# Optimization experiments

Measured on AMD Instinct MI355X. Metric: run time of the kernel, lower is better.

The kernel has to match this reference:

```python
import jax, jax.numpy as jnp
import numpy as np

MARGIN = 0.1

def setup_inputs() -> dict:
    key = jax.random.key(0)
    k1, k2 = jax.random.split(key)
    embeddings = jax.random.normal(k1, (8192, 128), dtype=jnp.float32)
    labels = jax.random.randint(k2, (8192,), 0, 64, dtype=jnp.int64)
    return {"embeddings": embeddings, "labels": labels}

def reference(embeddings, labels):
    # sim[i,j] = <e_i, e_j>
    sim = embeddings @ embeddings.T  # [n, n]
    eq = labels[:, None] == labels[None, :]  # pos mask (includes diagonal)
    # per entry: exp(margin - sim) for positives, exp(sim - margin) for negatives
    terms = jnp.where(eq, jnp.exp(MARGIN - sim), jnp.exp(sim - MARGIN))
    # loss_i = log(sum_j terms[i,j]); loss = mean_i loss_i
    return jnp.mean(jnp.log(jnp.sum(terms, axis=1)))
```

## Files before the change

kernel.cpp:

```cpp
#include <hip/hip_runtime.h>
#include <hip/hip_bf16.h>

#define N 8192
#define D 128
#define LOG2E  1.44269504088896f
#define LN2    0.69314718055995f

typedef __attribute__((ext_vector_type(8))) short bf16x8;
typedef __attribute__((ext_vector_type(4))) float f32x4;

#if __has_builtin(__builtin_amdgcn_exp2f)
#define EXP2(x) __builtin_amdgcn_exp2f(x)
#else
#define EXP2(x) exp2f(x)
#endif
#if __has_builtin(__builtin_amdgcn_logf)
#define LOG2(x) __builtin_amdgcn_logf(x)
#else
#define LOG2(x) log2f(x)
#endif

static __device__ __forceinline__ unsigned short f2bf(float f) {
    union { float f; unsigned int u; } x;
    x.f = f;
    unsigned int r = ((x.u >> 16) & 1u) + 0x7FFFu;
    return (unsigned short)((x.u + r) >> 16);
}

__global__ void prep_kernel(const float* __restrict__ E,
                            uint4* __restrict__ Eb2,
                            unsigned int* __restrict__ counter) {
    const int j = blockIdx.x * 256 + threadIdx.x;
    const int l  = j & 15;
    const int q  = (j >> 4) & 3;
    const int kk = (j >> 6) & 3;
    const int S  = j >> 8;
    const float4* src = (const float4*)(E + (size_t)(S * 16 + l) * D + kk * 32 + q * 8);
    float4 f0 = src[0], f1 = src[1];
    uint4 o;
    o.x = f2bf(f0.x) | ((unsigned)f2bf(f0.y) << 16);
    o.y = f2bf(f0.z) | ((unsigned)f2bf(f0.w) << 16);
    o.z = f2bf(f1.x) | ((unsigned)f2bf(f1.y) << 16);
    o.w = f2bf(f1.z) | ((unsigned)f2bf(f1.w) << 16);
    Eb2[j] = o;
    if (j == 0) *counter = 0u;
}

__global__ __launch_bounds__(256) void fused_kernel(
        const unsigned short* __restrict__ Eb2,
        const int* __restrict__ labels,
        float* __restrict__ part) {
    __shared__ int   labC[128];
    __shared__ int   labR[128];
    __shared__ float colacc[128];

    const int tid  = threadIdx.x;
    const int wid  = tid >> 6;
    const int lane = tid & 63;
    const int q = lane >> 4;
    const int l = lane & 15;

    const int b = blockIdx.x;
    int r = (int)(64.5f - sqrtf(64.5f * 64.5f - 2.0f * (float)b));
    while ((r + 1) * 64 - ((r + 1) * r) / 2 <= b) ++r;
    while (r * 64 - (r * (r - 1)) / 2 > b) --r;
    const int c = r + (b - (r * 64 - (r * (r - 1)) / 2));
    const bool diag = (r == c);
    const int tile_m0 = r * 128;
    const int n_begin = c * 128;
    const int mrow0 = wid * 32;

    const char* base = (const char*)Eb2;

    bf16x8 a[2][4];
#pragma unroll
    for (int g = 0; g < 2; ++g) {
        const char* pa = base + (size_t)(r * 8 + wid * 2 + g) * 4096 + lane * 16;
#pragma unroll
        for (int kk = 0; kk < 4; ++kk)
            a[g][kk] = *(const bf16x8*)(pa + kk * 1024);
    }

    if (tid < 128) { labC[tid] = labels[n_begin + tid]; colacc[tid] = 0.0f; }
    else           { labR[tid - 128] = labels[tile_m0 + (tid - 128)]; }
    __syncthreads();

    int lrow[8];
#pragma unroll
    for (int g = 0; g < 2; ++g)
#pragma unroll
        for (int rr = 0; rr < 4; ++rr)
            lrow[g * 4 + rr] = labR[mrow0 + g * 16 + q * 4 + rr];

    float sum[8];
#pragma unroll
    for (int i = 0; i < 8; ++i) sum[i] = 0.0f;

#pragma clang loop unroll(disable)
    for (int s = 0; s < 8; ++s) {
        const char* pb = base + (size_t)(c * 8 + s) * 4096 + lane * 16;
        bf16x8 b0 = *(const bf16x8*)(pb);
        bf16x8 b1 = *(const bf16x8*)(pb + 1024);
        bf16x8 b2 = *(const bf16x8*)(pb + 2048);
        bf16x8 b3 = *(const bf16x8*)(pb + 3072);
        const int lc = labC[s * 16 + l];

        f32x4 acc0 = (f32x4){0.f, 0.f, 0.f, 0.f};
        f32x4 acc1 = (f32x4){0.f, 0.f, 0.f, 0.f};
        acc0 = __builtin_amdgcn_mfma_f32_16x16x32_bf16(a[0][0], b0, acc0, 0, 0, 0);
        acc0 = __builtin_amdgcn_mfma_f32_16x16x32_bf16(a[0][1], b1, acc0, 0, 0, 0);
        acc0 = __builtin_amdgcn_mfma_f32_16x16x32_bf16(a[0][2], b2, acc0, 0, 0, 0);
        acc0 = __builtin_amdgcn_mfma_f32_16x16x32_bf16(a[0][3], b3, acc0, 0, 0, 0);
        acc1 = __builtin_amdgcn_mfma_f32_16x16x32_bf16(a[1][0], b0, acc1, 0, 0, 0);
        acc1 = __builtin_amdgcn_mfma_f32_16x16x32_bf16(a[1][1], b1, acc1, 0, 0, 0);
        acc1 = __builtin_amdgcn_mfma_f32_16x16x32_bf16(a[1][2], b2, acc1, 0, 0, 0);
        acc1 = __builtin_amdgcn_mfma_f32_16x16x32_bf16(a[1][3], b3, acc1, 0, 0, 0);

        float cp = 0.0f;
#pragma unroll
        for (int g = 0; g < 2; ++g) {
#pragma unroll
            for (int rr = 0; rr < 4; ++rr) {
                float sv = (g == 0) ? acc0[rr] : acc1[rr];
                bool eq = (lrow[g * 4 + rr] == lc);
                float cc = eq ? -LOG2E : LOG2E;
                float term = EXP2(cc * (sv - 0.1f));
                sum[g * 4 + rr] += term;
                cp += term;
            }
        }
        if (!diag) {
            cp += __shfl_xor(cp, 16);
            cp += __shfl_xor(cp, 32);
            if (q == 0) atomicAdd(&colacc[s * 16 + l], cp);
        }
    }

#pragma unroll
    for (int i = 0; i < 8; ++i) {
        float v = sum[i];
        v += __shfl_xor(v, 1);
        v += __shfl_xor(v, 2);
        v += __shfl_xor(v, 4);
        v += __shfl_xor(v, 8);
        sum[i] = v;
    }
    if (l == 0) {
#pragma unroll
        for (int g = 0; g < 2; ++g)
#pragma unroll
            for (int rr = 0; rr < 4; ++rr)
                part[(size_t)c * N + tile_m0 + mrow0 + g * 16 + q * 4 + rr] = sum[g * 4 + rr];
    }

    __syncthreads();
    if (!diag && tid < 128)
        part[(size_t)r * N + n_begin + tid] = colacc[tid];
}

__global__ void finalize_kernel(const float* __restrict__ part,
                                float* __restrict__ bpart,
                                unsigned int* __restrict__ counter,
                                float* __restrict__ out) {
    __shared__ float red[4];
    __shared__ unsigned int tk;
    const int tid = threadIdx.x;
    const int i = blockIdx.x * 256 + tid;

    float s = 0.0f;
#pragma unroll 8
    for (int x = 0; x < 64; ++x) s += part[(size_t)x * N + i];
    float v = LOG2(s) * LN2;
#pragma unroll
    for (int off = 1; off <= 32; off <<= 1) v += __shfl_xor(v, off);
    if ((tid & 63) == 0) red[tid >> 6] = v;
    __syncthreads();
    if (tid == 0) {
        bpart[blockIdx.x] = red[0] + red[1] + red[2] + red[3];
        __threadfence();
        tk = atomicAdd(counter, 1u);
    }
    __syncthreads();
    if (tk == 31u) {
        __threadfence();
        if (tid < 64) {
            float t = (tid < 32)
                ? __hip_atomic_load(&bpart[tid], __ATOMIC_RELAXED,
                                    __HIP_MEMORY_SCOPE_AGENT)
                : 0.0f;
#pragma unroll
            for (int off = 1; off <= 32; off <<= 1) t += __shfl_xor(t, off);
            if (tid == 0) out[0] = t * (1.0f / (float)N);
        }
    }
}

extern "C" void kernel_launch(void* const* d_in, const int* in_sizes, int n_in,
                              void* d_out, int out_size, void* d_ws, size_t ws_size,
                              hipStream_t stream) {
    const float* E = (const float*)d_in[0];
    const int* labels = (const int*)d_in[1];
    float* out = (float*)d_out;

    unsigned short* Eb2 = (unsigned short*)d_ws;
    float* part = (float*)((char*)d_ws + (size_t)N * D * 2);
    float* bpart = part + (size_t)64 * N;
    unsigned int* counter = (unsigned int*)(bpart + 32);

    prep_kernel<<<512, 256, 0, stream>>>(E, (uint4*)Eb2, counter);
    fused_kernel<<<2080, 256, 0, stream>>>(Eb2, labels, part);
    finalize_kernel<<<32, 256, 0, stream>>>(part, bpart, counter, out);
}
```

Baseline: 83.75 us.

## Fuse bf16 conversion into main kernel, dropping the prep pass

Removes the separate prep kernel that converted fp32 embeddings into a packed bf16 fragment layout. The fused kernel now reads fp32 rows directly and converts them to bf16 in registers with hardware pack intrinsics, and it also resets the counter itself. This saves one launch and a round trip through the workspace, but each tile now loads twice as many bytes from fp32 and converts them redundantly, since every B tile is reused by many blocks.

```diff
diff --git a/kernel.cpp b/kernel.cpp
--- a/kernel.cpp
+++ b/kernel.cpp
@@ -5,6 +5,7 @@
 #define D 128
 #define LOG2E  1.44269504088896f
 #define LN2    0.69314718055995f
+#define NPLANE 64
 
 typedef __attribute__((ext_vector_type(8))) short bf16x8;
 typedef __attribute__((ext_vector_type(4))) float f32x4;
@@ -20,36 +21,31 @@
 #define LOG2(x) log2f(x)
 #endif
 
-static __device__ __forceinline__ unsigned short f2bf(float f) {
-    union { float f; unsigned int u; } x;
-    x.f = f;
-    unsigned int r = ((x.u >> 16) & 1u) + 0x7FFFu;
-    return (unsigned short)((x.u + r) >> 16);
-}
-
-__global__ void prep_kernel(const float* __restrict__ E,
-                            uint4* __restrict__ Eb2,
-                            unsigned int* __restrict__ counter) {
-    const int j = blockIdx.x * 256 + threadIdx.x;
-    const int l  = j & 15;
-    const int q  = (j >> 4) & 3;
-    const int kk = (j >> 6) & 3;
-    const int S  = j >> 8;
-    const float4* src = (const float4*)(E + (size_t)(S * 16 + l) * D + kk * 32 + q * 8);
-    float4 f0 = src[0], f1 = src[1];
-    uint4 o;
-    o.x = f2bf(f0.x) | ((unsigned)f2bf(f0.y) << 16);
-    o.y = f2bf(f0.z) | ((unsigned)f2bf(f0.w) << 16);
-    o.z = f2bf(f1.x) | ((unsigned)f2bf(f1.y) << 16);
-    o.w = f2bf(f1.z) | ((unsigned)f2bf(f1.w) << 16);
-    Eb2[j] = o;
-    if (j == 0) *counter = 0u;
+union FragU { unsigned int u[4]; bf16x8 v; };
+
+static __device__ __forceinline__ unsigned int pk2(float x, float y) {
+    __hip_bfloat162 h = __float22bfloat162_rn(float2{x, y});
+    return *reinterpret_cast<unsigned int*>(&h);
+}
+
+static __device__ __forceinline__ bf16x8 load_frag(
+        const float* __restrict__ E, int row, int kk, int q) {
+    const float* p = E + (size_t)row * D + kk * 32 + q * 8;
+    float4 f0 = *(const float4*)p;
+    float4 f1 = *(const float4*)(p + 4);
+    FragU f;
+    f.u[0] = pk2(f0.x, f0.y);
+    f.u[1] = pk2(f0.z, f0.w);
+    f.u[2] = pk2(f1.x, f1.y);
+    f.u[3] = pk2(f1.z, f1.w);
+    return f.v;
 }
 
 __global__ __launch_bounds__(256) void fused_kernel(
-        const unsigned short* __restrict__ Eb2,
+        const float* __restrict__ E,
         const int* __restrict__ labels,
-        float* __restrict__ part) {
+        float* __restrict__ part,
+        unsigned int* __restrict__ counter) {
     __shared__ int   labC[128];
     __shared__ int   labR[128];
     __shared__ float colacc[128];
@@ -59,6 +55,8 @@
     const int lane = tid & 63;
     const int q = lane >> 4;
     const int l = lane & 15;
+
+    if (blockIdx.x == 0 && tid == 0) *counter = 0u;
 
     const int b = blockIdx.x;
     int r = (int)(64.5f - sqrtf(64.5f * 64.5f - 2.0f * (float)b));
@@ -70,16 +68,12 @@
     const int n_begin = c * 128;
     const int mrow0 = wid * 32;
 
-    const char* base = (const char*)Eb2;
-
     bf16x8 a[2][4];
 #pragma unroll
-    for (int g = 0; g < 2; ++g) {
-        const char* pa = base + (size_t)(r * 8 + wid * 2 + g) * 4096 + lane * 16;
+    for (int g = 0; g < 2; ++g)
 #pragma unroll
         for (int kk = 0; kk < 4; ++kk)
-            a[g][kk] = *(const bf16x8*)(pa + kk * 1024);
-    }
+            a[g][kk] = load_frag(E, tile_m0 + mrow0 + g * 16 + l, kk, q);
 
     if (tid < 128) { labC[tid] = labels[n_begin + tid]; colacc[tid] = 0.0f; }
     else           { labR[tid - 128] = labels[tile_m0 + (tid - 128)]; }
@@ -98,11 +92,11 @@
 
 #pragma clang loop unroll(disable)
     for (int s = 0; s < 8; ++s) {
-        const char* pb = base + (size_t)(c * 8 + s) * 4096 + lane * 16;
-        bf16x8 b0 = *(const bf16x8*)(pb);
-        bf16x8 b1 = *(const bf16x8*)(pb + 1024);
-        bf16x8 b2 = *(const bf16x8*)(pb + 2048);
-        bf16x8 b3 = *(const bf16x8*)(pb + 3072);
+        const int brow = n_begin + s * 16 + l;
+        bf16x8 b0 = load_frag(E, brow, 0, q);
+        bf16x8 b1 = load_frag(E, brow, 1, q);
+        bf16x8 b2 = load_frag(E, brow, 2, q);
+        bf16x8 b3 = load_frag(E, brow, 3, q);
         const int lc = labC[s * 16 + l];
 
         f32x4 acc0 = (f32x4){0.f, 0.f, 0.f, 0.f};
@@ -169,7 +163,7 @@
 
     float s = 0.0f;
 #pragma unroll 8
-    for (int x = 0; x < 64; ++x) s += part[(size_t)x * N + i];
+    for (int x = 0; x < NPLANE; ++x) s += part[(size_t)x * N + i];
     float v = LOG2(s) * LN2;
 #pragma unroll
     for (int off = 1; off <= 32; off <<= 1) v += __shfl_xor(v, off);
@@ -202,12 +196,10 @@
     const int* labels = (const int*)d_in[1];
     float* out = (float*)d_out;
 
-    unsigned short* Eb2 = (unsigned short*)d_ws;
-    float* part = (float*)((char*)d_ws + (size_t)N * D * 2);
-    float* bpart = part + (size_t)64 * N;
+    float* part = (float*)d_ws;
+    float* bpart = part + (size_t)NPLANE * N;
     unsigned int* counter = (unsigned int*)(bpart + 32);
 
-    prep_kernel<<<512, 256, 0, stream>>>(E, (uint4*)Eb2, counter);
-    fused_kernel<<<2080, 256, 0, stream>>>(Eb2, labels, part);
+    fused_kernel<<<2080, 256, 0, stream>>>(E, labels, part, counter);
     finalize_kernel<<<32, 256, 0, stream>>>(part, bpart, counter, out);
 }
```

New measurement: 142.3 us. +69.9%, slower.
